# Kernel tuning notes

Measured on AMD Instinct MI355X. Metric: run time of the kernel, lower is better.

## Reference

```python
import jax, jax.numpy as jnp
import numpy as np

N, E, B = 131072, 262144, 4096
NODE_DIM, EDGE_DIM, HIDDEN = 16, 4, 64
MLP_HID = 128


def setup_inputs() -> dict:
    key = jax.random.key(0)
    ks = jax.random.split(key, 16)
    def nrm(k, shape, s=0.05):
        return jax.random.normal(k, shape, jnp.float32) * s
    return {
        "x": jax.random.normal(ks[0], (N, NODE_DIM), jnp.float32),
        "edge_attr": jax.random.normal(ks[1], (E, EDGE_DIM), jnp.float32),
        "edge_index": jax.random.randint(ks[2], (2, E), 0, N),
        "batch": jnp.sort(jax.random.randint(ks[3], (N,), 0, B)),
        "w_e1": nrm(ks[4], (EDGE_DIM, MLP_HID)),
        "b_e1": jnp.zeros((MLP_HID,), jnp.float32),
        "w_e2": nrm(ks[5], (MLP_HID, NODE_DIM * HIDDEN)),
        "b_e2": jnp.zeros((NODE_DIM * HIDDEN,), jnp.float32),
        "root": nrm(ks[6], (NODE_DIM, HIDDEN)),
        "conv_bias": jnp.zeros((HIDDEN,), jnp.float32),
        "gru_wih": nrm(ks[7], (3 * HIDDEN, HIDDEN)),
        "gru_whh": nrm(ks[8], (3 * HIDDEN, HIDDEN)),
        "gru_bih": jnp.zeros((3 * HIDDEN,), jnp.float32),
        "gru_bhh": jnp.zeros((3 * HIDDEN,), jnp.float32),
        "lstm_wih": nrm(ks[9], (4 * HIDDEN, 2 * HIDDEN)),
        "lstm_whh": nrm(ks[10], (4 * HIDDEN, HIDDEN)),
        "lstm_bih": jnp.zeros((4 * HIDDEN,), jnp.float32),
        "lstm_bhh": jnp.zeros((4 * HIDDEN,), jnp.float32),
        "fc1_w": nrm(ks[11], (2 * HIDDEN, HIDDEN)),
        "fc1_b": jnp.zeros((HIDDEN,), jnp.float32),
        "fc2_w": nrm(ks[12], (HIDDEN, 1)),
        "fc2_b": jnp.zeros((1,), jnp.float32),
    }


def reference(x, edge_attr, edge_index, batch,
              w_e1, b_e1, w_e2, b_e2, root, conv_bias,
              gru_wih, gru_whh, gru_bih, gru_bhh,
              lstm_wih, lstm_whh, lstm_bih, lstm_bhh,
              fc1_w, fc1_b, fc2_w, fc2_b):
    src, dst = edge_index[0], edge_index[1]
    # NNConv: edge-MLP -> per-edge weight [E, node_dim, hidden]
    Wdyn = (jax.nn.relu(edge_attr @ w_e1 + b_e1) @ w_e2 + b_e2).reshape(E, NODE_DIM, HIDDEN)
    msg = jnp.einsum('ed,edh->eh', x[src], Wdyn)  # gather + per-edge matmul
    msum = jax.ops.segment_sum(msg, dst, num_segments=N)
    cnt = jax.ops.segment_sum(jnp.ones((E,), msg.dtype), dst, num_segments=N)
    agg = msum / jnp.maximum(cnt, 1.0)[:, None]  # scatter-mean
    out = jax.nn.relu(agg + x @ root + conv_bias)
    h = out
    for _ in range(3):
        gi = out @ gru_wih.T + gru_bih
        gh = h @ gru_whh.T + gru_bhh
        ir, iz, inn = jnp.split(gi, 3, axis=-1)
        hr, hz, hn = jnp.split(gh, 3, axis=-1)
        r = jax.nn.sigmoid(ir + hr)
        z = jax.nn.sigmoid(iz + hz)
        n = jnp.tanh(inn + r * hn)
        h = (1.0 - z) * n + z * h
        out = h
    # Set2Set, 3 processing steps
    hl = jnp.zeros((B, HIDDEN), out.dtype)
    cl = jnp.zeros((B, HIDDEN), out.dtype)
    q_star = jnp.zeros((B, 2 * HIDDEN), out.dtype)
    for _ in range(3):
        gates = q_star @ lstm_wih.T + lstm_bih + hl @ lstm_whh.T + lstm_bhh
        ig, fg, gg, og = jnp.split(gates, 4, axis=-1)
        ig = jax.nn.sigmoid(ig); fg = jax.nn.sigmoid(fg)
        gg = jnp.tanh(gg); og = jax.nn.sigmoid(og)
        cl = fg * cl + ig * gg
        hl = og * jnp.tanh(cl)
        q = hl  # [B, H]
        e = jnp.sum(out * q[batch], axis=-1)  # [N]
        m = jax.lax.stop_gradient(jax.ops.segment_max(e, batch, num_segments=B))
        ex = jnp.exp(e - m[batch])
        denom = jax.ops.segment_sum(ex, batch, num_segments=B)
        a = ex / denom[batch]  # segment softmax
        r_g = jax.ops.segment_sum(a[:, None] * out, batch, num_segments=B)
        q_star = jnp.concatenate([q, r_g], axis=-1)
    y = jax.nn.relu(q_star @ fc1_w + fc1_b)
    return (y @ fc2_w + fc2_b).squeeze(-1)
```

## Files before the change

kernel.cpp:

```cpp
#include <hip/hip_runtime.h>
#include <math.h>

#define N_NODES 131072
#define N_EDGES 262144
#define N_B     4096

typedef __attribute__((ext_vector_type(8))) short short8;
typedef __attribute__((ext_vector_type(8))) _Float16 half8;
typedef __attribute__((ext_vector_type(4))) float f32x4;
typedef __attribute__((ext_vector_type(16))) float f32x16;

__device__ __forceinline__ float fast_sig(float x) {
    return 1.0f / (1.0f + __expf(-x));
}
__device__ __forceinline__ float fast_tanh(float x) {
    float t = __expf(-2.0f * fabsf(x));
    float r = (1.0f - t) / (1.0f + t);
    return copysignf(r, x);
}

__device__ __forceinline__ void split_fp16(float v, _Float16& hi, _Float16& lo) {
    _Float16 h = (_Float16)v;
    hi = h;
    lo = (_Float16)(v - (float)h);
}

__global__ __launch_bounds__(256) void k_misc(
    const float* __restrict__ we2, unsigned short* __restrict__ wt,
    const float* __restrict__ gwih, const float* __restrict__ gwhh,
    const float* __restrict__ gbih, const float* __restrict__ gbhh,
    unsigned short* __restrict__ wtg, float* __restrict__ gbias,
    const float* __restrict__ lwih, const float* __restrict__ lwhh,
    float4* __restrict__ wA, float4* __restrict__ wB,
    const int* __restrict__ batch, int* __restrict__ starts)
{
    const int bid = blockIdx.x;
    const int tid = threadIdx.x;
    if (bid < 64) {
        int p = bid * 256 + tid;
        int d = p >> 10;
        int u = (p >> 9) & 1;
        int s = (p >> 6) & 7;
        int l = p & 63;
        int k0 = s * 16 + ((l >> 5) << 3);
        int h = u * 32 + (l & 31);
        half8 hv;
        #pragma unroll
        for (int j = 0; j < 8; ++j) {
            float v = we2[(size_t)(k0 + j) * 1024 + d * 64 + h];
            hv[j] = (_Float16)v;
        }
        size_t base = (size_t)d * 8192 + (size_t)u * 4096 + s * 512 + l * 8;
        *(half8*)&wt[base] = hv;
    } else if (bid < 72) {
        int p = (bid - 64) * 256 + tid;
        if (p < 256) {
            int g = p >> 6, j = p & 63;
            float b;
            if (g == 0)      b = gbih[j] + gbhh[j];
            else if (g == 1) b = gbih[64 + j] + gbhh[64 + j];
            else if (g == 2) b = gbih[128 + j];
            else             b = gbhh[128 + j];
            gbias[p] = b;
        }
        int u = p >> 7, ks = (p >> 6) & 1, ln = p & 63;
        int n = u * 16 + (ln & 15);
        int g = n >> 6, jn = n & 63;
        int k0 = ks * 32 + (ln >> 4) * 8;
        half8 hv;
        #pragma unroll
        for (int jj = 0; jj < 8; ++jj) {
            int k = k0 + jj;
            float v;
            if (g == 0)      v = gwih[jn * 64 + k] + gwhh[jn * 64 + k];
            else if (g == 1) v = gwih[(64 + jn) * 64 + k] + gwhh[(64 + jn) * 64 + k];
            else if (g == 2) v = gwih[(128 + jn) * 64 + k];
            else             v = gwhh[(128 + jn) * 64 + k];
            hv[jj] = (_Float16)v;
        }
        size_t base = (size_t)(u * 2 + ks) * 512 + ln * 8;
        *(half8*)&wtg[base] = hv;
    } else if (bid < 88) {
        int p = (bid - 72) * 256 + tid;
        int k = p >> 6, ln = p & 63;
        float4 a, b;
        a.x = lwih[(0 * 64 + ln) * 128 + k] + lwhh[(0 * 64 + ln) * 64 + k];
        a.y = lwih[(1 * 64 + ln) * 128 + k] + lwhh[(1 * 64 + ln) * 64 + k];
        a.z = lwih[(2 * 64 + ln) * 128 + k] + lwhh[(2 * 64 + ln) * 64 + k];
        a.w = lwih[(3 * 64 + ln) * 128 + k] + lwhh[(3 * 64 + ln) * 64 + k];
        b.x = lwih[(0 * 64 + ln) * 128 + 64 + k];
        b.y = lwih[(1 * 64 + ln) * 128 + 64 + k];
        b.z = lwih[(2 * 64 + ln) * 128 + 64 + k];
        b.w = lwih[(3 * 64 + ln) * 128 + 64 + k];
        wA[p] = a; wB[p] = b;
    } else {
        int g = (bid - 88) * 256 + tid;
        if (g > N_B) return;
        if (g == N_B) { starts[N_B] = N_NODES; return; }
        int lo = 0, hi = N_NODES;
        while (lo < hi) {
            int mid = (lo + hi) >> 1;
            if (batch[mid] < g) lo = mid + 1; else hi = mid;
        }
        starts[g] = lo;
    }
}

__global__ __launch_bounds__(256)
__attribute__((amdgpu_waves_per_eu(3, 4)))
void k_edge(
    const float* __restrict__ x,
    const float* __restrict__ ea,
    const int*   __restrict__ eidx,
    const float* __restrict__ we1,
    const float* __restrict__ be1,
    const unsigned short* __restrict__ wt,
    const float* __restrict__ be2,
    float* __restrict__ msum,
    float* __restrict__ cnt)
{
    __shared__ unsigned short sAh[16384];
    __shared__ float sxT[16 * 136];
    __shared__ float sbe2[1024];
    __shared__ int   sdst[128];

    const int tid = threadIdx.x;
    const int w   = tid >> 6;
    const int ln  = tid & 63;
    const int u     = w >> 1;
    const int mbase = (w & 1) * 2;
    const int eb  = blockIdx.x * 128;

    if (tid < 128) sdst[tid] = eidx[N_EDGES + eb + tid];
    #pragma unroll
    for (int v = tid; v < 1024; v += 256) sbe2[v] = be2[v];

    #pragma unroll
    for (int v = tid; v < 512; v += 256) {
        int e = v >> 2, q = v & 3;
        int src = eidx[eb + e];
        float4 t4 = ((const float4*)(x + (size_t)src * 16))[q];
        sxT[(q * 4 + 0) * 136 + e] = t4.x;
        sxT[(q * 4 + 1) * 136 + e] = t4.y;
        sxT[(q * 4 + 2) * 136 + e] = t4.z;
        sxT[(q * 4 + 3) * 136 + e] = t4.w;
    }

    #pragma unroll 1
    for (int i = 0; i < 8; ++i) {
        int cc = tid + i * 256;
        int mt = cc >> 9;
        int s  = (cc >> 6) & 7;
        int l  = cc & 63;
        int e   = mt * 32 + (l & 31);
        int kk0 = s * 16 + ((l >> 5) << 3);
        float4 eav = *(const float4*)(ea + (size_t)(eb + e) * 4);
        float4 b0 = *(const float4*)(be1 + kk0);
        float4 b1 = *(const float4*)(be1 + kk0 + 4);
        float acc[8] = {b0.x, b0.y, b0.z, b0.w, b1.x, b1.y, b1.z, b1.w};
        #pragma unroll
        for (int a = 0; a < 4; ++a) {
            float4 wa0 = *(const float4*)(we1 + a * 128 + kk0);
            float4 wa1 = *(const float4*)(we1 + a * 128 + kk0 + 4);
            float ev = (a == 0) ? eav.x : (a == 1) ? eav.y : (a == 2) ? eav.z : eav.w;
            acc[0] += ev * wa0.x; acc[1] += ev * wa0.y;
            acc[2] += ev * wa0.z; acc[3] += ev * wa0.w;
            acc[4] += ev * wa1.x; acc[5] += ev * wa1.y;
            acc[6] += ev * wa1.z; acc[7] += ev * wa1.w;
        }
        half8 hv;
        #pragma unroll
        for (int j = 0; j < 8; ++j) {
            hv[j] = (_Float16)fmaxf(acc[j], 0.0f);
        }
        *(half8*)&sAh[cc * 8] = hv;
    }
    __syncthreads();

    half8 ah[2][8];
    #pragma unroll
    for (int m2 = 0; m2 < 2; ++m2) {
        int mt = mbase + m2;
        #pragma unroll
        for (int s = 0; s < 8; ++s) {
            ah[m2][s] = *(half8*)&sAh[((mt * 8 + s) * 64 + ln) * 8];
        }
    }
    #pragma unroll
    for (int m2 = 0; m2 < 2; ++m2) {
        #pragma unroll
        for (int s = 0; s < 8; ++s) {
            asm volatile("" : "+v"(ah[m2][s]));
        }
    }

    const unsigned short* wdu = wt + (size_t)u * 4096;
    const int d0 = blockIdx.x & 15;
    const int rbase = (ln >> 5) * 4;

    f32x16 msg[2];
    #pragma unroll
    for (int r = 0; r < 16; ++r) { msg[0][r] = 0.0f; msg[1][r] = 0.0f; }

    half8 bq[8];
    {
        const unsigned short* p0 = wdu + (size_t)d0 * 8192 + ln * 8;
        #pragma unroll
        for (int f = 0; f < 7; ++f) bq[f] = *(const half8*)(p0 + f * 512);
    }

    #pragma unroll 1
    for (int dd = 0; dd < 16; ++dd) {
        const int d = (d0 + dd) & 15;
        const unsigned short* wd  = wdu + (size_t)d * 8192;
        const unsigned short* wnx = wdu + (size_t)((d + 1) & 15) * 8192;

        float bv = sbe2[d * 64 + u * 32 + (ln & 31)];
        f32x16 c2[2];
        #pragma unroll
        for (int r = 0; r < 16; ++r) { c2[0][r] = bv; c2[1][r] = bv; }

        #pragma unroll
        for (int s = 0; s < 8; ++s) {
            if (s == 0) {
                bq[7] = *(const half8*)(wd + 7 * 512 + ln * 8);
            } else if (dd < 15) {
                bq[s - 1] = *(const half8*)(wnx + (s - 1) * 512 + ln * 8);
            }
            half8 bb = bq[s];
            c2[0] = __builtin_amdgcn_mfma_f32_32x32x16_f16(ah[0][s], bb, c2[0], 0, 0, 0);
            c2[1] = __builtin_amdgcn_mfma_f32_32x32x16_f16(ah[1][s], bb, c2[1], 0, 0, 0);
        }
        #pragma unroll
        for (int m2 = 0; m2 < 2; ++m2) {
            #pragma unroll
            for (int q = 0; q < 4; ++q) {
                f32x4 xv = *(const f32x4*)&sxT[d * 136 + (mbase + m2) * 32 + rbase + 8 * q];
                #pragma unroll
                for (int j = 0; j < 4; ++j) {
                    msg[m2][q * 4 + j] = fmaf(xv[j], c2[m2][q * 4 + j], msg[m2][q * 4 + j]);
                }
            }
        }
    }

    const int col = u * 32 + (ln & 31);
    #pragma unroll
    for (int m2 = 0; m2 < 2; ++m2) {
        #pragma unroll
        for (int r = 0; r < 16; ++r) {
            int row = (r & 3) + ((r >> 2) * 8) + rbase;
            int dst = sdst[(mbase + m2) * 32 + row];
            atomicAdd(msum + (size_t)dst * 64 + col, msg[m2][r]);
        }
    }
    if (u == 0 && (ln & 31) == 0) {
        #pragma unroll
        for (int m2 = 0; m2 < 2; ++m2) {
            #pragma unroll
            for (int r = 0; r < 16; ++r) {
                int row = (r & 3) + ((r >> 2) * 8) + rbase;
                atomicAdd(&cnt[sdst[(mbase + m2) * 32 + row]], 1.0f);
            }
        }
    }
}

__global__ __launch_bounds__(256, 2) void k_gru2(
    float* __restrict__ buf,
    const float* __restrict__ cnt,
    const float* __restrict__ x,
    const float* __restrict__ root,
    const float* __restrict__ cb,
    const unsigned short* __restrict__ wtg,
    const float* __restrict__ gbias)
{
    __shared__ unsigned short sAh[16384];
    __shared__ unsigned short sAl[16384];
    __shared__ float sroot[1024];
    __shared__ float sbias[256];
    __shared__ float scb[64];
    const int tid = threadIdx.x;
    const int w = tid >> 6, ln = tid & 63, lq = ln >> 4, lm = ln & 15;
    const size_t nbase = (size_t)blockIdx.x * 256;

    #pragma unroll
    for (int v = tid; v < 1024; v += 256) sroot[v] = root[v];
    sbias[tid] = gbias[tid];
    if (tid < 64) scb[tid] = cb[tid];
    __syncthreads();

    #pragma unroll 1
    for (int i = 0; i < 8; ++i) {
        int cc = tid + i * 256;
        int mt = cc >> 7, ks = (cc >> 6) & 1, l = cc & 63;
        size_t gn = nbase + mt * 16 + (l & 15);
        int c0 = ks * 32 + (l >> 4) * 8;
        float4 m0 = *(const float4*)(buf + gn * 64 + c0);
        float4 m1 = *(const float4*)(buf + gn * 64 + c0 + 4);
        float cinv = 1.0f / fmaxf(cnt[gn], 1.0f);
        float xv[16];
        *(float4*)&xv[0]  = *(const float4*)(x + gn * 16);
        *(float4*)&xv[4]  = *(const float4*)(x + gn * 16 + 4);
        *(float4*)&xv[8]  = *(const float4*)(x + gn * 16 + 8);
        *(float4*)&xv[12] = *(const float4*)(x + gn * 16 + 12);
        float acc[8];
        #pragma unroll
        for (int j = 0; j < 8; ++j) acc[j] = scb[c0 + j];
        #pragma unroll
        for (int d = 0; d < 16; ++d) {
            float xd = xv[d];
            #pragma unroll
            for (int j = 0; j < 8; ++j) acc[j] += xd * sroot[d * 64 + c0 + j];
        }
        float ms[8] = {m0.x, m0.y, m0.z, m0.w, m1.x, m1.y, m1.z, m1.w};
        half8 hv, lv;
        #pragma unroll
        for (int j = 0; j < 8; ++j) {
            float hval = fmaxf(ms[j] * cinv + acc[j], 0.0f);
            _Float16 hi, lo; split_fp16(hval, hi, lo);
            hv[j] = hi; lv[j] = lo;
        }
        *(half8*)&sAh[cc * 8] = hv;
        *(half8*)&sAl[cc * 8] = lv;
    }
    __syncthreads();

    float hreg[4][4][4];
    #pragma unroll 1
    for (int step = 0; step < 3; ++step) {
        half8 ah[4][2], al[4][2];
        #pragma unroll
        for (int i = 0; i < 4; ++i)
            #pragma unroll
            for (int ks = 0; ks < 2; ++ks) {
                int mt = w * 4 + i;
                ah[i][ks] = *(half8*)&sAh[((mt * 2 + ks) * 64 + ln) * 8];
                al[i][ks] = *(half8*)&sAl[((mt * 2 + ks) * 64 + ln) * 8];
            }
        if (step == 0) {
            #pragma unroll
            for (int v = 0; v < 4; ++v) {
                int ksp = v >> 1;
                int lq2 = (v & 1) * 2 + (lm >> 3);
                int jp = lm & 7;
                #pragma unroll
                for (int i = 0; i < 4; ++i) {
                    int mt = w * 4 + i;
                    #pragma unroll
                    for (int r = 0; r < 4; ++r) {
                        int idx = ((mt * 2 + ksp) * 64 + lq2 * 16 + lq * 4 + r) * 8 + jp;
                        float hi = (float)*(const _Float16*)&sAh[idx];
                        float lo = (float)*(const _Float16*)&sAl[idx];
                        hreg[v][i][r] = hi + lo;
                    }
                }
            }
        }
        __syncthreads();

        #pragma unroll 1
        for (int v = 0; v < 4; ++v) {
            f32x4 C[4][4];
            #pragma unroll
            for (int g = 0; g < 4; ++g) {
                float bv = sbias[g * 64 + v * 16 + lm];
                #pragma unroll
                for (int i = 0; i < 4; ++i) C[g][i] = (f32x4){bv, bv, bv, bv};
            }
            #pragma unroll
            for (int g = 0; g < 4; ++g) {
                int u = g * 4 + v;
                #pragma unroll
                for (int ks = 0; ks < 2; ++ks) {
                    size_t wb = (size_t)(u * 2 + ks) * 512 + ln * 8;
                    half8 bb = *(const half8*)&wtg[wb];
                    #pragma unroll
                    for (int i = 0; i < 4; ++i) {
                        C[g][i] = __builtin_amdgcn_mfma_f32_16x16x32_f16(ah[i][ks], bb, C[g][i], 0, 0, 0);
                        C[g][i] = __builtin_amdgcn_mfma_f32_16x16x32_f16(al[i][ks], bb, C[g][i], 0, 0, 0);
                    }
                }
            }
            int ksp = v >> 1;
            int lq2 = (v & 1) * 2 + (lm >> 3);
            int jp = lm & 7;
            #pragma unroll
            for (int i = 0; i < 4; ++i) {
                int mt = w * 4 + i;
                #pragma unroll
                for (int r = 0; r < 4; ++r) {
                    float rr = fast_sig(C[0][i][r]);
                    float zz = fast_sig(C[1][i][r]);
                    float nn = fast_tanh(C[2][i][r] + rr * C[3][i][r]);
                    float hnew = (1.0f - zz) * nn + zz * hreg[v][i][r];
                    hreg[v][i][r] = hnew;
                    if (step < 2) {
                        _Float16 hi, lo; split_fp16(hnew, hi, lo);
                        int idx = ((mt * 2 + ksp) * 64 + lq2 * 16 + lq * 4 + r) * 8 + jp;
                        sAh[idx] = *(unsigned short*)&hi;
                        sAl[idx] = *(unsigned short*)&lo;
                    } else {
                        buf[(nbase + mt * 16 + lq * 4 + r) * 64 + v * 16 + lm] = hnew;
                    }
                }
            }
        }
        if (step < 2) __syncthreads();
    }
}

__global__ __launch_bounds__(256) void k_s2s(
    const float* __restrict__ out,
    const int*   __restrict__ starts,
    const float4* __restrict__ wA,
    const float4* __restrict__ wB,
    const float* __restrict__ bih,
    const float* __restrict__ bhh,
    const float* __restrict__ fc1w,
    const float* __restrict__ fc1b,
    const float* __restrict__ fc2w,
    const float* __restrict__ fc2b,
    float* __restrict__ y)
{
    __shared__ float osh[4][32][66];
    __shared__ float qsL[4][128];
    __shared__ float ebuf[4][256];
    const int tid = threadIdx.x;
    const int wv = tid >> 6, ln = tid & 63;
    const int gid = blockIdx.x * 4 + wv;

    const int s0 = starts[gid];
    int L = starts[gid + 1] - s0; if (L > 256) L = 256;
    const int SL = (L < 32) ? L : 32;

    #pragma unroll
    for (int base = 0; base < 32; base += 4) {
        int row = base + (ln >> 4);
        int c4 = (ln & 15) * 4;
        if (row < SL)
            *(float4*)&osh[wv][row][c4] =
                *(const float4*)(out + (size_t)(s0 + row) * 64 + c4);
    }

    qsL[wv][ln] = 0.0f; qsL[wv][64 + ln] = 0.0f;
    __builtin_amdgcn_wave_barrier();

    const float b0 = bih[ln] + bhh[ln];
    const float b1 = bih[64 + ln] + bhh[64 + ln];
    const float b2 = bih[128 + ln] + bhh[128 + ln];
    const float b3 = bih[192 + ln] + bhh[192 + ln];

    float c = 0.0f;

    #pragma unroll 1
    for (int step = 0; step < 3; ++step) {
        float a0 = b0, a1 = b1, a2 = b2, a3 = b3;
        #pragma unroll 4
        for (int k = 0; k < 64; ++k) {
            float qk = qsL[wv][k];
            float rk = qsL[wv][64 + k];
            float4 wa = wA[k * 64 + ln];
            float4 wb = wB[k * 64 + ln];
            a0 += wa.x * qk + wb.x * rk;
            a1 += wa.y * qk + wb.y * rk;
            a2 += wa.z * qk + wb.z * rk;
            a3 += wa.w * qk + wb.w * rk;
        }
        float ig = fast_sig(a0), fg = fast_sig(a1);
        float gg = fast_tanh(a2), og = fast_sig(a3);
        c = fg * c + ig * gg;
        float h = og * fast_tanh(c);
        __builtin_amdgcn_wave_barrier();
        qsL[wv][ln] = h;
        __builtin_amdgcn_wave_barrier();

        float m = -1e30f;
        for (int c0 = 0; c0 * 64 < L; ++c0) {
            int j = c0 * 64 + ln;
            if (j < L) {
                float a = 0.0f;
                if (j < SL) {
                    #pragma unroll
                    for (int l4 = 0; l4 < 16; ++l4) {
                        float4 ov = *(const float4*)&osh[wv][j][l4 * 4];
                        float4 hv = *(const float4*)&qsL[wv][l4 * 4];
                        a += ov.x * hv.x + ov.y * hv.y + ov.z * hv.z + ov.w * hv.w;
                    }
                } else {
                    const float4* orow = (const float4*)(out + (size_t)(s0 + j) * 64);
                    #pragma unroll
                    for (int l4 = 0; l4 < 16; ++l4) {
                        float4 ov = orow[l4];
                        float4 hv = *(const float4*)&qsL[wv][l4 * 4];
                        a += ov.x * hv.x + ov.y * hv.y + ov.z * hv.z + ov.w * hv.w;
                    }
                }
                ebuf[wv][j] = a;
                m = fmaxf(m, a);
            }
        }
        #pragma unroll
        for (int off = 32; off; off >>= 1) m = fmaxf(m, __shfl_xor(m, off));
        float ds = 0.0f;
        for (int c0 = 0; c0 * 64 < L; ++c0) {
            int j = c0 * 64 + ln;
            if (j < L) {
                float ex = __expf(ebuf[wv][j] - m);
                ebuf[wv][j] = ex;
                ds += ex;
            }
        }
        #pragma unroll
        for (int off = 32; off; off >>= 1) ds += __shfl_xor(ds, off);
        __builtin_amdgcn_wave_barrier();
        float rg = 0.0f;
        for (int j = 0; j < SL; ++j)
            rg = fmaf(ebuf[wv][j], osh[wv][j][ln], rg);
        for (int j = SL; j < L; ++j)
            rg = fmaf(ebuf[wv][j], out[(size_t)(s0 + j) * 64 + ln], rg);
        rg = (L > 0) ? (rg / ds) : 0.0f;
        qsL[wv][64 + ln] = rg;
        __builtin_amdgcn_wave_barrier();
    }

    float a = fc1b[ln];
    #pragma unroll 4
    for (int k = 0; k < 128; ++k)
        a = fmaf(qsL[wv][k], fc1w[k * 64 + ln], a);
    float uu = fmaxf(a, 0.0f) * fc2w[ln];
    #pragma unroll
    for (int off = 32; off; off >>= 1) uu += __shfl_xor(uu, off);
    if (ln == 0) y[gid] = uu + fc2b[0];
}

extern "C" void kernel_launch(void* const* d_in, const int* in_sizes, int n_in,
                              void* d_out, int out_size, void* d_ws, size_t ws_size,
                              hipStream_t stream) {
    const float* x     = (const float*)d_in[0];
    const float* ea    = (const float*)d_in[1];
    const int*   eidx  = (const int*)d_in[2];
    const int*   batch = (const int*)d_in[3];
    const float* we1   = (const float*)d_in[4];
    const float* be1   = (const float*)d_in[5];
    const float* we2   = (const float*)d_in[6];
    const float* be2   = (const float*)d_in[7];
    const float* root  = (const float*)d_in[8];
    const float* cb    = (const float*)d_in[9];
    const float* gwih  = (const float*)d_in[10];
    const float* gwhh  = (const float*)d_in[11];
    const float* gbih  = (const float*)d_in[12];
    const float* gbhh  = (const float*)d_in[13];
    const float* lwih  = (const float*)d_in[14];
    const float* lwhh  = (const float*)d_in[15];
    const float* lbih  = (const float*)d_in[16];
    const float* lbhh  = (const float*)d_in[17];
    const float* fc1w  = (const float*)d_in[18];
    const float* fc1b  = (const float*)d_in[19];
    const float* fc2w  = (const float*)d_in[20];
    const float* fc2b  = (const float*)d_in[21];

    float* buf = (float*)d_ws;
    float* cnt = buf + (size_t)N_NODES * 64;
    int* starts = (int*)(cnt + N_NODES);
    size_t off = ((size_t)N_NODES * 64 + N_NODES + N_B + 1) * 4;
    off = (off + 15) & ~(size_t)15;
    unsigned short* wt  = (unsigned short*)((char*)d_ws + off);
    unsigned short* wtg = wt + 262144;
    float* gbias = (float*)(wtg + 32768);
    float4* wA = (float4*)(gbias + 256);
    float4* wB = wA + 4096;
    float* y = (float*)d_out;

    hipMemsetAsync(d_ws, 0, ((size_t)N_NODES * 64 + N_NODES) * sizeof(float), stream);
    k_misc<<<105, 256, 0, stream>>>(we2, wt, gwih, gwhh, gbih, gbhh, wtg, gbias,
                                    lwih, lwhh, wA, wB, batch, starts);
    k_edge<<<N_EDGES / 128, 256, 0, stream>>>(x, ea, eidx, we1, be1, wt, be2, buf, cnt);
    k_gru2<<<N_NODES / 256, 256, 0, stream>>>(buf, cnt, x, root, cb, wtg, gbias);
    k_s2s<<<N_B / 4, 256, 0, stream>>>(buf, starts, wA, wB, lbih, lbhh,
                                       fc1w, fc1b, fc2w, fc2b, y);
}
```

Baseline: 403.5 us.

## Replace atomic scatter-mean with CSR build and gather-based aggregation

```diff
diff --git a/kernel.cpp b/kernel.cpp
--- a/kernel.cpp
+++ b/kernel.cpp
@@ -32,10 +32,16 @@
     unsigned short* __restrict__ wtg, float* __restrict__ gbias,
     const float* __restrict__ lwih, const float* __restrict__ lwhh,
     float4* __restrict__ wA, float4* __restrict__ wB,
-    const int* __restrict__ batch, int* __restrict__ starts)
+    const int* __restrict__ batch, int* __restrict__ starts,
+    const int* __restrict__ eidx, int* __restrict__ deg)
 {
     const int bid = blockIdx.x;
     const int tid = threadIdx.x;
+    if (bid >= 105) {
+        int p = (bid - 105) * 256 + tid;
+        atomicAdd(&deg[eidx[N_EDGES + p]], 1);
+        return;
+    }
     if (bid < 64) {
         int p = bid * 256 + tid;
         int d = p >> 10;
@@ -106,6 +112,71 @@
     }
 }
 
+__global__ __launch_bounds__(256) void k_scan1(
+    const int* __restrict__ deg, int* __restrict__ psum)
+{
+    __shared__ int sm[256];
+    const int t = threadIdx.x;
+    sm[t] = deg[blockIdx.x * 256 + t];
+    __syncthreads();
+    #pragma unroll
+    for (int off = 128; off; off >>= 1) {
+        if (t < off) sm[t] += sm[t + off];
+        __syncthreads();
+    }
+    if (t == 0) psum[blockIdx.x] = sm[0];
+}
+
+__global__ __launch_bounds__(512) void k_scan2(
+    const int* __restrict__ psum, int* __restrict__ psumx)
+{
+    __shared__ int sm[512];
+    const int t = threadIdx.x;
+    sm[t] = psum[t];
+    __syncthreads();
+    #pragma unroll
+    for (int off = 1; off < 512; off <<= 1) {
+        int add = (t >= off) ? sm[t - off] : 0;
+        __syncthreads();
+        sm[t] += add;
+        __syncthreads();
+    }
+    psumx[t] = (t > 0) ? sm[t - 1] : 0;
+}
+
+__global__ __launch_bounds__(256) void k_scan3(
+    const int* __restrict__ deg, const int* __restrict__ psumx,
+    int* __restrict__ row_ptr, int* __restrict__ cursor)
+{
+    __shared__ int sm[256];
+    const int t = threadIdx.x;
+    const int i = blockIdx.x * 256 + t;
+    int d = deg[i];
+    sm[t] = d;
+    __syncthreads();
+    #pragma unroll
+    for (int off = 1; off < 256; off <<= 1) {
+        int add = (t >= off) ? sm[t - off] : 0;
+        __syncthreads();
+        sm[t] += add;
+        __syncthreads();
+    }
+    int excl = sm[t] - d + psumx[blockIdx.x];
+    row_ptr[i] = excl;
+    cursor[i] = excl;
+    if (i == 0) row_ptr[N_NODES] = N_EDGES;
+}
+
+__global__ __launch_bounds__(256) void k_scat(
+    const int* __restrict__ eidx, int* __restrict__ cursor,
+    int* __restrict__ eord)
+{
+    int e = blockIdx.x * 256 + threadIdx.x;
+    int dst = eidx[N_EDGES + e];
+    int pos = atomicAdd(&cursor[dst], 1);
+    eord[pos] = e;
+}
+
 __global__ __launch_bounds__(256)
 __attribute__((amdgpu_waves_per_eu(3, 4)))
 void k_edge(
@@ -116,13 +187,11 @@
     const float* __restrict__ be1,
     const unsigned short* __restrict__ wt,
     const float* __restrict__ be2,
-    float* __restrict__ msum,
-    float* __restrict__ cnt)
+    float* __restrict__ emsg)
 {
     __shared__ unsigned short sAh[16384];
     __shared__ float sxT[16 * 136];
     __shared__ float sbe2[1024];
-    __shared__ int   sdst[128];
 
     const int tid = threadIdx.x;
     const int w   = tid >> 6;
@@ -131,7 +200,6 @@
     const int mbase = (w & 1) * 2;
     const int eb  = blockIdx.x * 128;
 
-    if (tid < 128) sdst[tid] = eidx[N_EDGES + eb + tid];
     #pragma unroll
     for (int v = tid; v < 1024; v += 256) sbe2[v] = be2[v];
 
@@ -250,25 +318,16 @@
         #pragma unroll
         for (int r = 0; r < 16; ++r) {
             int row = (r & 3) + ((r >> 2) * 8) + rbase;
-            int dst = sdst[(mbase + m2) * 32 + row];
-            atomicAdd(msum + (size_t)dst * 64 + col, msg[m2][r]);
-        }
-    }
-    if (u == 0 && (ln & 31) == 0) {
-        #pragma unroll
-        for (int m2 = 0; m2 < 2; ++m2) {
-            #pragma unroll
-            for (int r = 0; r < 16; ++r) {
-                int row = (r & 3) + ((r >> 2) * 8) + rbase;
-                atomicAdd(&cnt[sdst[(mbase + m2) * 32 + row]], 1.0f);
-            }
+            emsg[(size_t)(eb + (mbase + m2) * 32 + row) * 64 + col] = msg[m2][r];
         }
     }
 }
 
 __global__ __launch_bounds__(256, 2) void k_gru2(
     float* __restrict__ buf,
-    const float* __restrict__ cnt,
+    const float* __restrict__ emsg,
+    const int* __restrict__ rowp,
+    const int* __restrict__ eord,
     const float* __restrict__ x,
     const float* __restrict__ root,
     const float* __restrict__ cb,
@@ -290,15 +349,22 @@
     if (tid < 64) scb[tid] = cb[tid];
     __syncthreads();
 
-    #pragma unroll 1
+    #pragma unroll 2
     for (int i = 0; i < 8; ++i) {
         int cc = tid + i * 256;
         int mt = cc >> 7, ks = (cc >> 6) & 1, l = cc & 63;
         size_t gn = nbase + mt * 16 + (l & 15);
         int c0 = ks * 32 + (l >> 4) * 8;
-        float4 m0 = *(const float4*)(buf + gn * 64 + c0);
-        float4 m1 = *(const float4*)(buf + gn * 64 + c0 + 4);
-        float cinv = 1.0f / fmaxf(cnt[gn], 1.0f);
+        int rp0 = rowp[gn], rp1 = rowp[gn + 1];
+        float ms[8] = {0.f, 0.f, 0.f, 0.f, 0.f, 0.f, 0.f, 0.f};
+        for (int k = rp0; k < rp1; ++k) {
+            int e = eord[k];
+            float4 m0 = *(const float4*)(emsg + (size_t)e * 64 + c0);
+            float4 m1 = *(const float4*)(emsg + (size_t)e * 64 + c0 + 4);
+            ms[0] += m0.x; ms[1] += m0.y; ms[2] += m0.z; ms[3] += m0.w;
+            ms[4] += m1.x; ms[5] += m1.y; ms[6] += m1.z; ms[7] += m1.w;
+        }
+        float cinv = 1.0f / fmaxf((float)(rp1 - rp0), 1.0f);
         float xv[16];
         *(float4*)&xv[0]  = *(const float4*)(x + gn * 16);
         *(float4*)&xv[4]  = *(const float4*)(x + gn * 16 + 4);
@@ -313,7 +379,6 @@
             #pragma unroll
             for (int j = 0; j < 8; ++j) acc[j] += xd * sroot[d * 64 + c0 + j];
         }
-        float ms[8] = {m0.x, m0.y, m0.z, m0.w, m1.x, m1.y, m1.z, m1.w};
         half8 hv, lv;
         #pragma unroll
         for (int j = 0; j < 8; ++j) {
@@ -560,10 +625,16 @@
     const float* fc2w  = (const float*)d_in[20];
     const float* fc2b  = (const float*)d_in[21];
 
-    float* buf = (float*)d_ws;
-    float* cnt = buf + (size_t)N_NODES * 64;
-    int* starts = (int*)(cnt + N_NODES);
-    size_t off = ((size_t)N_NODES * 64 + N_NODES + N_B + 1) * 4;
+    float* emsg = (float*)d_ws;
+    float* buf  = emsg + (size_t)N_EDGES * 64;
+    int* deg    = (int*)(buf + (size_t)N_NODES * 64);
+    int* rowp   = deg + N_NODES;
+    int* cursor = rowp + N_NODES + 1;
+    int* eord   = cursor + N_NODES;
+    int* psum   = eord + N_EDGES;
+    int* psumx  = psum + 512;
+    int* starts = psumx + 512;
+    size_t off = (size_t)((char*)(starts + N_B + 1) - (char*)d_ws);
     off = (off + 15) & ~(size_t)15;
     unsigned short* wt  = (unsigned short*)((char*)d_ws + off);
     unsigned short* wtg = wt + 262144;
@@ -572,11 +643,16 @@
     float4* wB = wA + 4096;
     float* y = (float*)d_out;
 
-    hipMemsetAsync(d_ws, 0, ((size_t)N_NODES * 64 + N_NODES) * sizeof(float), stream);
-    k_misc<<<105, 256, 0, stream>>>(we2, wt, gwih, gwhh, gbih, gbhh, wtg, gbias,
-                                    lwih, lwhh, wA, wB, batch, starts);
-    k_edge<<<N_EDGES / 128, 256, 0, stream>>>(x, ea, eidx, we1, be1, wt, be2, buf, cnt);
-    k_gru2<<<N_NODES / 256, 256, 0, stream>>>(buf, cnt, x, root, cb, wtg, gbias);
+    hipMemsetAsync(deg, 0, (size_t)N_NODES * sizeof(int), stream);
+    k_misc<<<1129, 256, 0, stream>>>(we2, wt, gwih, gwhh, gbih, gbhh, wtg, gbias,
+                                     lwih, lwhh, wA, wB, batch, starts, eidx, deg);
+    k_scan1<<<512, 256, 0, stream>>>(deg, psum);
+    k_scan2<<<1, 512, 0, stream>>>(psum, psumx);
+    k_scan3<<<512, 256, 0, stream>>>(deg, psumx, rowp, cursor);
+    k_scat<<<1024, 256, 0, stream>>>(eidx, cursor, eord);
+    k_edge<<<N_EDGES / 128, 256, 0, stream>>>(x, ea, eidx, we1, be1, wt, be2, emsg);
+    k_gru2<<<N_NODES / 256, 256, 0, stream>>>(buf, emsg, rowp, eord, x, root, cb,
+                                              wtg, gbias);
     k_s2s<<<N_B / 4, 256, 0, stream>>>(buf, starts, wA, wB, lbih, lbhh,
                                        fc1w, fc1b, fc2w, fc2b, y);
 }
```

After: 424.8 us. 1.05x slower.
